# Performance work log

Measured on AMD Instinct MI355X. Metric: run time of the kernel, lower is better.

Reference implementation:

```python
import jax, jax.numpy as jnp
import numpy as np

B, F, S, D = 8, 4, 512, 256
H, DK, DV = 8, 32, 32
LN_EPS = 1e-5


def setup_inputs() -> dict:
    key = jax.random.key(0)
    ks = jax.random.split(key, 8)
    scale = 1.0 / np.sqrt(D)
    return {
        "x": jax.random.normal(ks[0], (B, F, S, D), dtype=jnp.float32),
        "res_att": jax.random.normal(ks[1], (B, F, H, S, S), dtype=jnp.float32),
        # weights stored as [in, out] (transpose of torch Linear.weight)
        "W_Q": jax.random.normal(ks[2], (D, H * DK), dtype=jnp.float32) * scale,
        "W_K": jax.random.normal(ks[3], (D, H * DK), dtype=jnp.float32) * scale,
        "W_V": jax.random.normal(ks[4], (D, H * DV), dtype=jnp.float32) * scale,
        "W_fc": jax.random.normal(ks[5], (H * DV, D), dtype=jnp.float32) * scale,
        "ln_g": jnp.ones((D,), dtype=jnp.float32),
        "ln_b": jnp.zeros((D,), dtype=jnp.float32),
    }


def _layer_norm(x, g, b):
    mu = jnp.mean(x, axis=-1, keepdims=True)
    var = jnp.var(x, axis=-1, keepdims=True)
    return (x - mu) * jax.lax.rsqrt(var + LN_EPS) * g + b


def reference(x, res_att, W_Q, W_K, W_V, W_fc, ln_g, ln_b):
    # x: [B, F, S, D]; project and split heads -> [B, F, H, S, dk]
    q = (x @ W_Q).reshape(B, F, S, H, DK).transpose(0, 1, 3, 2, 4)
    k = (x @ W_K).reshape(B, F, S, H, DK).transpose(0, 1, 3, 2, 4)
    v = (x @ W_V).reshape(B, F, S, H, DV).transpose(0, 1, 3, 2, 4)
    # RealFormer-style residual attention bias
    scores = jnp.einsum("bfhsk,bfhtk->bfhst", q, k) / np.sqrt(DK) + res_att
    # NOTE: original uses F.softmax(scores, dim=3) -> over the QUERY axis
    attn = jax.nn.softmax(scores, axis=3)
    ctx = jnp.einsum("bfhst,bfhtv->bfhsv", attn, v)
    ctx = ctx.transpose(0, 1, 3, 2, 4).reshape(B, F, S, H * DV)
    out = ctx @ W_fc
    out = _layer_norm(out + x, ln_g, ln_b)
    return out, scores
```

## Files before the change

### kernel.cpp

```cpp
#include <hip/hip_runtime.h>
#include <math.h>

#define B_   8
#define F_   4
#define S_   512
#define D_   256
#define H_   8
#define DK_  32
#define DV_  32
#define NBF  32
#define NROWS (NBF * S_)
#define NG   (NBF * H_)
#define LN_EPS 1e-5f

typedef __attribute__((ext_vector_type(8))) short bf16x8;
typedef __attribute__((ext_vector_type(4))) float f32x4;
typedef __attribute__((ext_vector_type(8))) unsigned short u16x8;

__device__ __forceinline__ short f2bf(float f) {
    union { float f; unsigned u; } v; v.f = f;
    unsigned u = v.u;
    u += 0x7FFFu + ((u >> 16) & 1u);
    return (short)(u >> 16);
}

__device__ __forceinline__ bf16x8 pack8(float4 a, float4 b) {
    bf16x8 r;
    r[0] = f2bf(a.x); r[1] = f2bf(a.y); r[2] = f2bf(a.z); r[3] = f2bf(a.w);
    r[4] = f2bf(b.x); r[5] = f2bf(b.y); r[6] = f2bf(b.z); r[7] = f2bf(b.w);
    return r;
}

__device__ __forceinline__ bf16x8 pack8v(f32x4 a, f32x4 b) {
    bf16x8 r;
    r[0] = f2bf(a[0]); r[1] = f2bf(a[1]); r[2] = f2bf(a[2]); r[3] = f2bf(a[3]);
    r[4] = f2bf(b[0]); r[5] = f2bf(b[1]); r[6] = f2bf(b[2]); r[7] = f2bf(b[3]);
    return r;
}

union BFU { u16x8 u; bf16x8 b; };

__global__ __launch_bounds__(64) void wpack_kernel(
    const float* __restrict__ Wq, const float* __restrict__ Wk,
    const float* __restrict__ Wv,
    unsigned short* __restrict__ Wp)
{
    const int bid  = blockIdx.x;
    const int ct   = bid & 15;
    const int ks   = (bid >> 4) & 7;
    const int wsel = bid >> 7;
    const float* W = (wsel == 0) ? Wq : (wsel == 1) ? Wk : Wv;
    const int lane = threadIdx.x;
    const int lr = lane & 15, lg = lane >> 4;
    u16x8 t;
#pragma unroll
    for (int j = 0; j < 8; ++j)
        t[j] = (unsigned short)f2bf(W[(ks * 32 + lg * 8 + j) * 256 + ct * 16 + lr]);
    *(u16x8*)(Wp + ((size_t)bid * 64 + lane) * 8) = t;
}

__global__ __launch_bounds__(256) void qkv_kernel(
    const float* __restrict__ x, const unsigned short* __restrict__ Wp,
    float* __restrict__ qo, float* __restrict__ ko, float* __restrict__ vo)
{
    const int bid    = blockIdx.x;
    const int rowblk = bid & 255;
    const int wsel   = bid >> 8;
    float* outp = (wsel == 0) ? qo : (wsel == 1) ? ko : vo;
    const int m0   = rowblk * 64;
    const int w    = threadIdx.x >> 6;
    const int lane = threadIdx.x & 63;
    const int lr = lane & 15, lg = lane >> 4;
    const int arow = m0 + w * 16 + lr;

    const f32x4 zero = {0.f, 0.f, 0.f, 0.f};
    f32x4 acc[16];
#pragma unroll
    for (int ct = 0; ct < 16; ++ct) acc[ct] = zero;

    for (int ks = 0; ks < 8; ++ks) {
        const float* xp = &x[(size_t)arow * 256 + ks * 32 + lg * 8];
        bf16x8 a = pack8(*(const float4*)xp, *(const float4*)(xp + 4));
        const u16x8* wp = (const u16x8*)(Wp + ((size_t)(wsel * 8 + ks) * 16) * 64 * 8);
#pragma unroll
        for (int ct = 0; ct < 16; ++ct) {
            BFU bb; bb.u = wp[ct * 64 + lane];
            acc[ct] = __builtin_amdgcn_mfma_f32_16x16x32_bf16(a, bb.b, acc[ct], 0, 0, 0);
        }
    }
#pragma unroll
    for (int ct = 0; ct < 16; ++ct)
#pragma unroll
        for (int j = 0; j < 4; ++j)
            outp[(size_t)(m0 + w * 16 + lg * 4 + j) * 256 + ct * 16 + lr] = acc[ct][j];
}

__global__ __launch_bounds__(512) void scores_kernel(
    const float* __restrict__ q, const float* __restrict__ k,
    const float* __restrict__ res, float* __restrict__ sc_out,
    float* __restrict__ pmax, float* __restrict__ psum)
{
    const int bid  = blockIdx.x;
    const int g    = bid & 255;
    const int st   = bid >> 8;
    const int bf = g >> 3, h = g & 7;
    const size_t qkbase = (size_t)bf * S_ * D_ + (size_t)h * 32;
    const size_t sbase  = (size_t)g * S_ * S_;
    const int s0 = st * 64;

    __shared__ float T[64][260];
    const int tid = threadIdx.x;
    const int w = tid >> 6, lane = tid & 63;
    const int lr = lane & 15, lg = lane >> 4;

    bf16x8 afrag[4];
#pragma unroll
    for (int rt = 0; rt < 4; ++rt) {
        const float* qp = &q[qkbase + (size_t)(s0 + rt * 16 + lr) * D_ + lg * 8];
        afrag[rt] = pack8(*(const float4*)qp, *(const float4*)(qp + 4));
    }

    const float scale = 0.17677669529663687f;
    const f32x4 zero = {0.f, 0.f, 0.f, 0.f};

    for (int ch = 0; ch < 2; ++ch) {
        const int c0 = ch * 256;
        __syncthreads();

#pragma unroll
        for (int p = 0; p < 8; ++p) {
            int idx = tid + p * 512;
            int r = idx >> 6, c4 = (idx & 63) * 4;
            const f32x4* rp =
                (const f32x4*)&res[sbase + (size_t)(s0 + r) * S_ + c0 + c4];
            *(f32x4*)&T[r][c4] = __builtin_nontemporal_load(rp);
        }
        __syncthreads();

#pragma unroll
        for (int ctl = 0; ctl < 2; ++ctl) {
            const int lcol = w * 32 + ctl * 16 + lr;
            const int tcol = c0 + lcol;
            const float* kp = &k[qkbase + (size_t)tcol * D_ + lg * 8];
            bf16x8 b = pack8(*(const float4*)kp, *(const float4*)(kp + 4));

            f32x4 accr[4];
#pragma unroll
            for (int rt = 0; rt < 4; ++rt)
                accr[rt] = __builtin_amdgcn_mfma_f32_16x16x32_bf16(afrag[rt], b, zero, 0, 0, 0);

            float sc[16];
#pragma unroll
            for (int rt = 0; rt < 4; ++rt)
#pragma unroll
                for (int j = 0; j < 4; ++j) {
                    const int r = rt * 16 + lg * 4 + j;
                    float v = fmaf(accr[rt][j], scale, T[r][lcol]);
                    T[r][lcol] = v;
                    sc[rt * 4 + j] = v;
                }
            float m = sc[0];
#pragma unroll
            for (int i = 1; i < 16; ++i) m = fmaxf(m, sc[i]);
            float z = 0.f;
#pragma unroll
            for (int i = 0; i < 16; ++i) z += __expf(sc[i] - m);
#pragma unroll
            for (int off = 16; off <= 32; off <<= 1) {
                float om = __shfl_xor(m, off);
                float oz = __shfl_xor(z, off);
                float nm = fmaxf(m, om);
                z = z * __expf(m - nm) + oz * __expf(om - nm);
                m = nm;
            }
            if (lg == 0) {
                pmax[((size_t)g * 8 + st) * S_ + tcol] = m;
                psum[((size_t)g * 8 + st) * S_ + tcol] = z;
            }
        }
        __syncthreads();

#pragma unroll
        for (int p = 0; p < 8; ++p) {
            int idx = tid + p * 512;
            int r = idx >> 6, c4 = (idx & 63) * 4;
            *(float4*)&sc_out[sbase + (size_t)(s0 + r) * S_ + c0 + c4] =
                *(float4*)&T[r][c4];
        }
    }
}

__global__ __launch_bounds__(256) void stats_kernel(
    const float* __restrict__ pmax, const float* __restrict__ psum,
    float* __restrict__ M, float* __restrict__ iZ)
{
    const int idx = blockIdx.x * 256 + threadIdx.x;
    const int g = idx >> 9;
    const int t = idx & 511;
    float m = -1e30f;
    float pm[8];
#pragma unroll
    for (int i = 0; i < 8; ++i) {
        pm[i] = pmax[((size_t)g * 8 + i) * S_ + t];
        m = fmaxf(m, pm[i]);
    }
    float z = 0.f;
#pragma unroll
    for (int i = 0; i < 8; ++i)
        z += psum[((size_t)g * 8 + i) * S_ + t] * __expf(pm[i] - m);
    M[idx]  = m;
    iZ[idx] = 1.f / z;
}

__global__ __launch_bounds__(256) void pv_kernel(
    const float* __restrict__ sc, const float* __restrict__ v,
    const float* __restrict__ M, const float* __restrict__ iZ,
    float* __restrict__ ctx)
{
    const int bid = blockIdx.x;
    const int g   = bid & 255;
    const int rt  = 7 - (bid >> 8);
    const int bf = g >> 3, h = g & 7;
    const size_t sbase = (size_t)g * S_ * S_;

    __shared__ unsigned short VT[32][520];
    __shared__ float Ml[S_];
    __shared__ float iZl[S_];
    const int tid = threadIdx.x;

    for (int i = tid; i < S_; i += 256) {
        Ml[i]  = M[(size_t)g * S_ + i];
        iZl[i] = iZ[(size_t)g * S_ + i];
    }
    for (int i = tid; i < S_ * 8; i += 256) {
        int t = i >> 3, v4 = (i & 7) * 4;
        float4 vv = *(const float4*)&v[((size_t)bf * S_ + t) * D_ + h * 32 + v4];
        VT[v4 + 0][t] = (unsigned short)f2bf(vv.x);
        VT[v4 + 1][t] = (unsigned short)f2bf(vv.y);
        VT[v4 + 2][t] = (unsigned short)f2bf(vv.z);
        VT[v4 + 3][t] = (unsigned short)f2bf(vv.w);
    }
    __syncthreads();

    const int w = tid >> 6, lane = tid & 63;
    const int lr = lane & 15, lg = lane >> 4;
    const int srow = rt * 64 + w * 16 + lr;

    const f32x4 zero = {0.f, 0.f, 0.f, 0.f};
    f32x4 acc[2] = {zero, zero};

    for (int kt = 0; kt < 16; ++kt) {
        const int t0 = kt * 32 + lg * 8;
        const float* sp = &sc[sbase + (size_t)srow * S_ + t0];
        f32x4 sa = __builtin_nontemporal_load((const f32x4*)sp);
        f32x4 sb = __builtin_nontemporal_load((const f32x4*)(sp + 4));
        bf16x8 a;
        a[0] = f2bf(__expf(sa[0] - Ml[t0 + 0]) * iZl[t0 + 0]);
        a[1] = f2bf(__expf(sa[1] - Ml[t0 + 1]) * iZl[t0 + 1]);
        a[2] = f2bf(__expf(sa[2] - Ml[t0 + 2]) * iZl[t0 + 2]);
        a[3] = f2bf(__expf(sa[3] - Ml[t0 + 3]) * iZl[t0 + 3]);
        a[4] = f2bf(__expf(sb[0] - Ml[t0 + 4]) * iZl[t0 + 4]);
        a[5] = f2bf(__expf(sb[1] - Ml[t0 + 5]) * iZl[t0 + 5]);
        a[6] = f2bf(__expf(sb[2] - Ml[t0 + 6]) * iZl[t0 + 6]);
        a[7] = f2bf(__expf(sb[3] - Ml[t0 + 7]) * iZl[t0 + 7]);
#pragma unroll
        for (int ct = 0; ct < 2; ++ct) {
            BFU bb;
            bb.u = *(u16x8*)&VT[ct * 16 + lr][kt * 32 + lg * 8];
            acc[ct] = __builtin_amdgcn_mfma_f32_16x16x32_bf16(a, bb.b, acc[ct], 0, 0, 0);
        }
    }
#pragma unroll
    for (int ct = 0; ct < 2; ++ct)
#pragma unroll
        for (int j = 0; j < 4; ++j)
            ctx[((size_t)bf * S_ + rt * 64 + w * 16 + lg * 4 + j) * D_
                + h * 32 + ct * 16 + lr] = acc[ct][j];
}

__global__ __launch_bounds__(256) void out_kernel(
    const float* __restrict__ ctx, const float* __restrict__ x,
    const float* __restrict__ Wfc, const float* __restrict__ gam,
    const float* __restrict__ bet, float* __restrict__ out)
{
    const int TM = 16;
    __shared__ float cs[TM][D_];
    __shared__ float red[TM][4][2];
    const int r0 = blockIdx.x * TM;
    const int j  = threadIdx.x;

    for (int i = threadIdx.x; i < TM * D_ / 4; i += 256) {
        int r = i / (D_ / 4);
        int c = (i % (D_ / 4)) * 4;
        *(float4*)&cs[r][c] = *(const float4*)&ctx[(size_t)(r0 + r) * D_ + c];
    }
    __syncthreads();

    float y[TM];
#pragma unroll
    for (int r = 0; r < TM; ++r) y[r] = 0.f;

    for (int kk = 0; kk < D_; kk += 4) {
        float w0 = Wfc[(kk + 0) * D_ + j], w1 = Wfc[(kk + 1) * D_ + j];
        float w2 = Wfc[(kk + 2) * D_ + j], w3 = Wfc[(kk + 3) * D_ + j];
#pragma unroll
        for (int r = 0; r < TM; ++r) {
            float4 c4 = *(const float4*)&cs[r][kk];
            y[r] = fmaf(c4.x, w0, y[r]); y[r] = fmaf(c4.y, w1, y[r]);
            y[r] = fmaf(c4.z, w2, y[r]); y[r] = fmaf(c4.w, w3, y[r]);
        }
    }
#pragma unroll
    for (int r = 0; r < TM; ++r) y[r] += x[(size_t)(r0 + r) * D_ + j];

    const int lane = threadIdx.x & 63;
    const int w    = threadIdx.x >> 6;
#pragma unroll
    for (int r = 0; r < TM; ++r) {
        float s1 = y[r], s2 = y[r] * y[r];
        for (int off = 32; off; off >>= 1) {
            s1 += __shfl_xor(s1, off);
            s2 += __shfl_xor(s2, off);
        }
        if (lane == 0) { red[r][w][0] = s1; red[r][w][1] = s2; }
    }
    __syncthreads();

#pragma unroll
    for (int r = 0; r < TM; ++r) {
        float s1 = red[r][0][0] + red[r][1][0] + red[r][2][0] + red[r][3][0];
        float s2 = red[r][0][1] + red[r][1][1] + red[r][2][1] + red[r][3][1];
        float mu  = s1 * (1.f / D_);
        float var = s2 * (1.f / D_) - mu * mu;
        float o = (y[r] - mu) * rsqrtf(var + LN_EPS) * gam[j] + bet[j];
        out[(size_t)(r0 + r) * D_ + j] = o;
    }
}

extern "C" void kernel_launch(void* const* d_in, const int* in_sizes, int n_in,
                              void* d_out, int out_size, void* d_ws, size_t ws_size,
                              hipStream_t stream)
{
    const float* x   = (const float*)d_in[0];
    const float* res = (const float*)d_in[1];
    const float* Wq  = (const float*)d_in[2];
    const float* Wk  = (const float*)d_in[3];
    const float* Wv  = (const float*)d_in[4];
    const float* Wfc = (const float*)d_in[5];
    const float* gam = (const float*)d_in[6];
    const float* bet = (const float*)d_in[7];

    float* out    = (float*)d_out;
    float* scores = out + (size_t)NROWS * D_;

    float* q    = (float*)d_ws;
    float* k    = q    + (size_t)NROWS * D_;
    float* v    = k    + (size_t)NROWS * D_;
    float* ctx  = v    + (size_t)NROWS * D_;
    float* pmax = ctx  + (size_t)NROWS * D_;
    float* psum = pmax + (size_t)NG * 8 * S_;
    float* M    = psum + (size_t)NG * 8 * S_;
    float* iZ   = M    + (size_t)NG * S_;
    unsigned short* Wp = (unsigned short*)ctx;

    wpack_kernel<<<dim3(384), 64, 0, stream>>>(Wq, Wk, Wv, Wp);
    qkv_kernel<<<dim3(768), 256, 0, stream>>>(x, Wp, q, k, v);
    scores_kernel<<<dim3(2048), 512, 0, stream>>>(q, k, res, scores, pmax, psum);
    stats_kernel<<<dim3(NG * S_ / 256), 256, 0, stream>>>(pmax, psum, M, iZ);
    pv_kernel<<<dim3(2048), 256, 0, stream>>>(scores, v, M, iZ, ctx);
    out_kernel<<<dim3(NROWS / 16), 256, 0, stream>>>(ctx, x, Wfc, gam, bet, out);
}
```

Before: 286.6 us.

## Compute output projection with bf16 MFMA using prepacked Wfc

The output projection moves from a scalar fp32 FMA loop to bf16 MFMA instructions. Wfc is now prepacked alongside the QKV weights, and the packed buffer moves to its own workspace region so it is not overwritten by ctx. Each block handles 64 rows and stages the projection result in shared memory before a per-16-row LayerNorm. The aim is to cut the FMA-bound cost of the final GEMM, at the price of bf16 rounding of ctx and Wfc and a large shared-memory tile that may limit occupancy.

```diff
diff --git a/kernel.cpp b/kernel.cpp
--- a/kernel.cpp
+++ b/kernel.cpp
@@ -31,25 +31,18 @@
     return r;
 }
 
-__device__ __forceinline__ bf16x8 pack8v(f32x4 a, f32x4 b) {
-    bf16x8 r;
-    r[0] = f2bf(a[0]); r[1] = f2bf(a[1]); r[2] = f2bf(a[2]); r[3] = f2bf(a[3]);
-    r[4] = f2bf(b[0]); r[5] = f2bf(b[1]); r[6] = f2bf(b[2]); r[7] = f2bf(b[3]);
-    return r;
-}
-
 union BFU { u16x8 u; bf16x8 b; };
 
 __global__ __launch_bounds__(64) void wpack_kernel(
     const float* __restrict__ Wq, const float* __restrict__ Wk,
-    const float* __restrict__ Wv,
+    const float* __restrict__ Wv, const float* __restrict__ Wfc,
     unsigned short* __restrict__ Wp)
 {
     const int bid  = blockIdx.x;
     const int ct   = bid & 15;
     const int ks   = (bid >> 4) & 7;
     const int wsel = bid >> 7;
-    const float* W = (wsel == 0) ? Wq : (wsel == 1) ? Wk : Wv;
+    const float* W = (wsel == 0) ? Wq : (wsel == 1) ? Wk : (wsel == 2) ? Wv : Wfc;
     const int lane = threadIdx.x;
     const int lr = lane & 15, lg = lane >> 4;
     u16x8 t;
@@ -280,60 +273,69 @@
 
 __global__ __launch_bounds__(256) void out_kernel(
     const float* __restrict__ ctx, const float* __restrict__ x,
-    const float* __restrict__ Wfc, const float* __restrict__ gam,
+    const unsigned short* __restrict__ Wp, const float* __restrict__ gam,
     const float* __restrict__ bet, float* __restrict__ out)
 {
-    const int TM = 16;
-    __shared__ float cs[TM][D_];
-    __shared__ float red[TM][4][2];
-    const int r0 = blockIdx.x * TM;
-    const int j  = threadIdx.x;
-
-    for (int i = threadIdx.x; i < TM * D_ / 4; i += 256) {
-        int r = i / (D_ / 4);
-        int c = (i % (D_ / 4)) * 4;
-        *(float4*)&cs[r][c] = *(const float4*)&ctx[(size_t)(r0 + r) * D_ + c];
-    }
+    __shared__ float Tl[64][260];
+    __shared__ float red[16][4][2];
+    const int m0   = blockIdx.x * 64;
+    const int tid  = threadIdx.x;
+    const int w    = tid >> 6;
+    const int lane = tid & 63;
+    const int lr = lane & 15, lg = lane >> 4;
+    const int arow = m0 + w * 16 + lr;
+
+    const f32x4 zero = {0.f, 0.f, 0.f, 0.f};
+    f32x4 acc[16];
+#pragma unroll
+    for (int ct = 0; ct < 16; ++ct) acc[ct] = zero;
+
+    for (int ks = 0; ks < 8; ++ks) {
+        const float* cp = &ctx[(size_t)arow * 256 + ks * 32 + lg * 8];
+        bf16x8 a = pack8(*(const float4*)cp, *(const float4*)(cp + 4));
+        const u16x8* wp = (const u16x8*)(Wp + ((size_t)(3 * 8 + ks) * 16) * 64 * 8);
+#pragma unroll
+        for (int ct = 0; ct < 16; ++ct) {
+            BFU bb; bb.u = wp[ct * 64 + lane];
+            acc[ct] = __builtin_amdgcn_mfma_f32_16x16x32_bf16(a, bb.b, acc[ct], 0, 0, 0);
+        }
+    }
+#pragma unroll
+    for (int ct = 0; ct < 16; ++ct)
+#pragma unroll
+        for (int j = 0; j < 4; ++j)
+            Tl[w * 16 + lg * 4 + j][ct * 16 + lr] = acc[ct][j];
     __syncthreads();
 
-    float y[TM];
-#pragma unroll
-    for (int r = 0; r < TM; ++r) y[r] = 0.f;
-
-    for (int kk = 0; kk < D_; kk += 4) {
-        float w0 = Wfc[(kk + 0) * D_ + j], w1 = Wfc[(kk + 1) * D_ + j];
-        float w2 = Wfc[(kk + 2) * D_ + j], w3 = Wfc[(kk + 3) * D_ + j];
-#pragma unroll
-        for (int r = 0; r < TM; ++r) {
-            float4 c4 = *(const float4*)&cs[r][kk];
-            y[r] = fmaf(c4.x, w0, y[r]); y[r] = fmaf(c4.y, w1, y[r]);
-            y[r] = fmaf(c4.z, w2, y[r]); y[r] = fmaf(c4.w, w3, y[r]);
-        }
-    }
-#pragma unroll
-    for (int r = 0; r < TM; ++r) y[r] += x[(size_t)(r0 + r) * D_ + j];
-
-    const int lane = threadIdx.x & 63;
-    const int w    = threadIdx.x >> 6;
-#pragma unroll
-    for (int r = 0; r < TM; ++r) {
-        float s1 = y[r], s2 = y[r] * y[r];
-        for (int off = 32; off; off >>= 1) {
-            s1 += __shfl_xor(s1, off);
-            s2 += __shfl_xor(s2, off);
-        }
-        if (lane == 0) { red[r][w][0] = s1; red[r][w][1] = s2; }
-    }
-    __syncthreads();
-
-#pragma unroll
-    for (int r = 0; r < TM; ++r) {
-        float s1 = red[r][0][0] + red[r][1][0] + red[r][2][0] + red[r][3][0];
-        float s2 = red[r][0][1] + red[r][1][1] + red[r][2][1] + red[r][3][1];
-        float mu  = s1 * (1.f / D_);
-        float var = s2 * (1.f / D_) - mu * mu;
-        float o = (y[r] - mu) * rsqrtf(var + LN_EPS) * gam[j] + bet[j];
-        out[(size_t)(r0 + r) * D_ + j] = o;
+    const int j = tid;
+    for (int rq = 0; rq < 4; ++rq) {
+        if (rq) __syncthreads();
+        const int r0 = m0 + rq * 16;
+        float y[16];
+#pragma unroll
+        for (int r = 0; r < 16; ++r)
+            y[r] = Tl[rq * 16 + r][j] + x[(size_t)(r0 + r) * D_ + j];
+
+#pragma unroll
+        for (int r = 0; r < 16; ++r) {
+            float s1 = y[r], s2 = y[r] * y[r];
+            for (int off = 32; off; off >>= 1) {
+                s1 += __shfl_xor(s1, off);
+                s2 += __shfl_xor(s2, off);
+            }
+            if (lane == 0) { red[r][w][0] = s1; red[r][w][1] = s2; }
+        }
+        __syncthreads();
+
+#pragma unroll
+        for (int r = 0; r < 16; ++r) {
+            float s1 = red[r][0][0] + red[r][1][0] + red[r][2][0] + red[r][3][0];
+            float s2 = red[r][0][1] + red[r][1][1] + red[r][2][1] + red[r][3][1];
+            float mu  = s1 * (1.f / D_);
+            float var = s2 * (1.f / D_) - mu * mu;
+            float o = (y[r] - mu) * rsqrtf(var + LN_EPS) * gam[j] + bet[j];
+            out[(size_t)(r0 + r) * D_ + j] = o;
+        }
     }
 }
 
@@ -361,12 +363,12 @@
     float* psum = pmax + (size_t)NG * 8 * S_;
     float* M    = psum + (size_t)NG * 8 * S_;
     float* iZ   = M    + (size_t)NG * S_;
-    unsigned short* Wp = (unsigned short*)ctx;
-
-    wpack_kernel<<<dim3(384), 64, 0, stream>>>(Wq, Wk, Wv, Wp);
+    unsigned short* Wp = (unsigned short*)(iZ + (size_t)NG * S_);
+
+    wpack_kernel<<<dim3(512), 64, 0, stream>>>(Wq, Wk, Wv, Wfc, Wp);
     qkv_kernel<<<dim3(768), 256, 0, stream>>>(x, Wp, q, k, v);
     scores_kernel<<<dim3(2048), 512, 0, stream>>>(q, k, res, scores, pmax, psum);
     stats_kernel<<<dim3(NG * S_ / 256), 256, 0, stream>>>(pmax, psum, M, iZ);
     pv_kernel<<<dim3(2048), 256, 0, stream>>>(scores, v, M, iZ, ctx);
-    out_kernel<<<dim3(NROWS / 16), 256, 0, stream>>>(ctx, x, Wfc, gam, bet, out);
-}
+    out_kernel<<<dim3(256), 256, 0, stream>>>(ctx, x, Wp, gam, bet, out);
+}
```

After: 262.4 us. -8.5%, faster.
